# Optimization experiments

Hardware: AMD Instinct MI355X
Metric: run time of the kernel (lower is better)

## Reference

```python
import jax, jax.numpy as jnp
import numpy as np

HIDDEN = 4096
N_HEADS = 32
N_KV_HEADS = 8
HEAD_DIM = 128
ROPE_THETA = 1e6
RMS_EPS = 1e-6
SEQ = 2048


def setup_inputs() -> dict:
    key = jax.random.key(0)
    k1, k2, k3 = jax.random.split(key, 3)
    hidden_states = jax.random.normal(k1, (SEQ, HIDDEN), dtype=jnp.float32)
    # fused QKV weight: [hidden, (H + 2*Hkv) * head_dim]
    qkv_out = (N_HEADS + 2 * N_KV_HEADS) * HEAD_DIM
    w_qkv = jax.random.normal(k2, (HIDDEN, qkv_out), dtype=jnp.float32) * (HIDDEN ** -0.5)
    w_o = jax.random.normal(k3, (N_HEADS * HEAD_DIM, HIDDEN), dtype=jnp.float32) * ((N_HEADS * HEAD_DIM) ** -0.5)
    q_norm_w = jnp.ones((HEAD_DIM,), dtype=jnp.float32)
    k_norm_w = jnp.ones((HEAD_DIM,), dtype=jnp.float32)
    # NeoX-style rotary tables [T, head_dim/2]
    pos = jnp.arange(SEQ, dtype=jnp.float32)
    inv_freq = 1.0 / (ROPE_THETA ** (jnp.arange(0, HEAD_DIM, 2, dtype=jnp.float32) / HEAD_DIM))
    freqs = pos[:, None] * inv_freq[None, :]  # [T, d/2]
    cos = jnp.cos(freqs)
    sin = jnp.sin(freqs)
    return {"hidden_states": hidden_states, "cos": cos, "sin": sin,
            "w_qkv": w_qkv, "w_o": w_o, "q_norm_w": q_norm_w, "k_norm_w": k_norm_w}


def _rms_norm(x, w, eps=RMS_EPS):
    # per-head RMSNorm over last dim (head_dim)
    var = jnp.mean(jnp.square(x), axis=-1, keepdims=True)
    return x * jax.lax.rsqrt(var + eps) * w


def _rope(x, cos, sin):
    # NeoX rotate-half: x split into two halves of head_dim
    d2 = x.shape[-1] // 2
    x1, x2 = x[..., :d2], x[..., d2:]
    c = cos[:, None, :]  # [T,1,d/2] broadcast over heads
    s = sin[:, None, :]
    return jnp.concatenate([x1 * c - x2 * s, x2 * c + x1 * s], axis=-1)


def reference(hidden_states, cos, sin, w_qkv, w_o, q_norm_w, k_norm_w):
    T = hidden_states.shape[0]
    H, Hkv, D = N_HEADS, N_KV_HEADS, HEAD_DIM
    G = H // Hkv  # GQA group size
    scale = D ** -0.5

    qkv = hidden_states @ w_qkv  # [T, (H+2Hkv)*D]
    q, k, v = jnp.split(qkv, [H * D, (H + Hkv) * D], axis=1)
    q = q.reshape(T, H, D)
    k = k.reshape(T, Hkv, D)
    v = v.reshape(T, Hkv, D)

    q = _rms_norm(q, q_norm_w)
    k = _rms_norm(k, k_norm_w)
    q = _rope(q, cos, sin)
    k = _rope(k, cos, sin)

    # GQA: group query heads onto shared KV heads
    qg = q.reshape(T, Hkv, G, D)
    scores = jnp.einsum('qhgd,khd->hgqk', qg, k) * scale  # [Hkv,G,T,T]
    causal = jnp.tril(jnp.ones((T, T), dtype=bool))
    scores = jnp.where(causal, scores, jnp.float32(-1e30))
    probs = jax.nn.softmax(scores, axis=-1)
    out = jnp.einsum('hgqk,khd->qhgd', probs, v).reshape(T, H * D)
    return out @ w_o  # [T, hidden]
```

## Files before the change

kernel.cpp:

```cpp
#include <hip/hip_runtime.h>
#include <stdint.h>

#define SEQ   2048
#define HID   4096
#define NQH   32
#define NKVH  8
#define HD    128
#define QKVN  6144

typedef uint16_t u16;
typedef __attribute__((ext_vector_type(8))) short bf16x8;
typedef __attribute__((ext_vector_type(4))) float f32x4;
typedef __attribute__((ext_vector_type(4))) unsigned int u32x4;

static __device__ __forceinline__ float bf2f(u16 h){
  union { float f; unsigned int u; } v; v.u = ((unsigned int)h) << 16; return v.f;
}
static __device__ __forceinline__ u16 f2bf(float f){
  unsigned int u = __float_as_uint(f);
  return (u16)((u + 0x7fffu + ((u >> 16) & 1u)) >> 16);
}
static __device__ __forceinline__ f32x4 mfma16(bf16x8 a, bf16x8 b, f32x4 c){
  return __builtin_amdgcn_mfma_f32_16x16x32_bf16(a, b, c, 0, 0, 0);
}
static __device__ __forceinline__ void gload16(const void* g, void* l){
  __builtin_amdgcn_global_load_lds((const __attribute__((address_space(1))) void*)g,
                                   (__attribute__((address_space(3))) void*)l, 16, 0, 0);
}

__global__ void k_cvt(const float* __restrict__ src, u16* __restrict__ dst, int n4){
  int i = blockIdx.x * blockDim.x + threadIdx.x;
  if (i >= n4) return;
  float4 v = ((const float4*)src)[i];
  uint2 o;
  o.x = (unsigned)f2bf(v.x) | ((unsigned)f2bf(v.y) << 16);
  o.y = (unsigned)f2bf(v.z) | ((unsigned)f2bf(v.w) << 16);
  ((uint2*)dst)[i] = o;
}

__global__ void k_addf(const float* __restrict__ a, float* __restrict__ o, int n4){
  int i = blockIdx.x * blockDim.x + threadIdx.x;
  if (i >= n4) return;
  float4 x = ((const float4*)o)[i];
  float4 y = ((const float4*)a)[i];
  x.x += y.x; x.y += y.y; x.z += y.z; x.w += y.w;
  ((float4*)o)[i] = x;
}

__global__ void k_transpose_cvt(const float* __restrict__ src, u16* __restrict__ dst, int K, int N){
  __shared__ float t[32][33];
  int n0 = blockIdx.x * 32, k0 = blockIdx.y * 32;
  int tx = threadIdx.x, ty = threadIdx.y;
#pragma unroll
  for (int i = 0; i < 32; i += 8)
    t[ty + i][tx] = src[(size_t)(k0 + ty + i) * N + n0 + tx];
  __syncthreads();
#pragma unroll
  for (int i = 0; i < 32; i += 8)
    dst[(size_t)(n0 + ty + i) * K + k0 + tx] = f2bf(t[tx][ty + i]);
}

template<int OUTBF, int SPLITK, int XBC, int NBY>
__global__ __launch_bounds__(512) void k_gemm(const u16* __restrict__ A, const u16* __restrict__ Bt,
                                              void* __restrict__ Cv0, void* __restrict__ Cv1,
                                              int M, int N, int K){
  __shared__ __align__(16) u16 Asm[2][256][64];
  __shared__ __align__(16) u16 Bsm[2][256][64];
  const int tid = threadIdx.x, lane = tid & 63, wid = tid >> 6;
  const int wm = wid >> 2, wn = wid & 3;
  const int l16 = lane & 15, lhi = lane >> 4;
  const int rx = l16 & 7;
  const int bid = blockIdx.x;
  const int xcd = bid & 7, j = bid >> 3;
  const int bcol_i = xcd * XBC + j % XBC;
  const int rest = j / XBC;
  const int brow_i = rest % NBY;
  const int kz = (SPLITK > 1) ? (rest / NBY) : 0;
  const size_t brow = (size_t)brow_i * 256, bcol = (size_t)bcol_i * 256;
  const int kbeg = kz * (K / SPLITK);
  void* Cv = (kz == 0) ? Cv0 : Cv1;

  const f32x4 vz = {0.f, 0.f, 0.f, 0.f};
  f32x4 acc[8][4];
#pragma unroll
  for (int m = 0; m < 8; m++)
#pragma unroll
    for (int n = 0; n < 4; n++) acc[m][n] = vz;

  const int srow = lane >> 3;
  const int sg   = (lane & 7) ^ srow;
  const u16* Ags = A  + (brow + wid*8 + srow) * (size_t)K + sg*8 + kbeg;
  const u16* Bgs = Bt + (bcol + wid*8 + srow) * (size_t)K + sg*8 + kbeg;
  const int NT = (K / SPLITK) >> 6;

#pragma unroll
  for (int j2 = 0; j2 < 4; j2++) gload16(Ags + (size_t)j2*64*K, &Asm[0][wid*8 + j2*64][0]);
#pragma unroll
  for (int j2 = 0; j2 < 4; j2++) gload16(Bgs + (size_t)j2*64*K, &Bsm[0][wid*8 + j2*64][0]);
  asm volatile("s_waitcnt vmcnt(0)" ::: "memory");
  __builtin_amdgcn_sched_barrier(0);
  __builtin_amdgcn_s_barrier();

  for (int t = 0; t < NT; ++t){
    const int cur = t & 1, nxt = cur ^ 1;
    const size_t ko = (size_t)(t + 1) * 64;
    const bool st = (t + 1 < NT);
    bf16x8 a[8], b0, b1, b2, b3;
#pragma unroll
    for (int mi = 0; mi < 8; ++mi)
      a[mi] = *(const bf16x8*)&Asm[cur][wm*128 + mi*16 + l16][(lhi ^ rx) << 3];
    b0 = *(const bf16x8*)&Bsm[cur][wn*64 +  0 + l16][(lhi ^ rx) << 3];
    b1 = *(const bf16x8*)&Bsm[cur][wn*64 + 16 + l16][(lhi ^ rx) << 3];
    if (st){
      gload16(Ags + ko,                  &Asm[nxt][wid*8      ][0]);
      gload16(Ags + (size_t)64*K + ko,   &Asm[nxt][wid*8 +  64][0]);
      gload16(Bgs + ko,                  &Bsm[nxt][wid*8      ][0]);
      gload16(Bgs + (size_t)64*K + ko,   &Bsm[nxt][wid*8 +  64][0]);
    }
    __builtin_amdgcn_s_barrier();
    asm volatile("s_waitcnt lgkmcnt(0)" ::: "memory");
    __builtin_amdgcn_sched_barrier(0);
    __builtin_amdgcn_s_setprio(1);
#pragma unroll
    for (int mi = 0; mi < 8; ++mi){
      acc[mi][0] = mfma16(a[mi], b0, acc[mi][0]);
      acc[mi][1] = mfma16(a[mi], b1, acc[mi][1]);
    }
    __builtin_amdgcn_s_setprio(0);
    __builtin_amdgcn_s_barrier();
    b2 = *(const bf16x8*)&Bsm[cur][wn*64 + 32 + l16][(lhi ^ rx) << 3];
    b3 = *(const bf16x8*)&Bsm[cur][wn*64 + 48 + l16][(lhi ^ rx) << 3];
    if (st){
      gload16(Ags + (size_t)128*K + ko,  &Asm[nxt][wid*8 + 128][0]);
      gload16(Ags + (size_t)192*K + ko,  &Asm[nxt][wid*8 + 192][0]);
      gload16(Bgs + (size_t)128*K + ko,  &Bsm[nxt][wid*8 + 128][0]);
      gload16(Bgs + (size_t)192*K + ko,  &Bsm[nxt][wid*8 + 192][0]);
    }
    __builtin_amdgcn_s_barrier();
    asm volatile("s_waitcnt lgkmcnt(0)" ::: "memory");
    __builtin_amdgcn_sched_barrier(0);
    __builtin_amdgcn_s_setprio(1);
#pragma unroll
    for (int mi = 0; mi < 8; ++mi){
      acc[mi][2] = mfma16(a[mi], b2, acc[mi][2]);
      acc[mi][3] = mfma16(a[mi], b3, acc[mi][3]);
    }
    __builtin_amdgcn_s_setprio(0);
    __builtin_amdgcn_s_barrier();
#pragma unroll
    for (int mi = 0; mi < 8; ++mi)
      a[mi] = *(const bf16x8*)&Asm[cur][wm*128 + mi*16 + l16][((4 + lhi) ^ rx) << 3];
    b0 = *(const bf16x8*)&Bsm[cur][wn*64 +  0 + l16][((4 + lhi) ^ rx) << 3];
    b1 = *(const bf16x8*)&Bsm[cur][wn*64 + 16 + l16][((4 + lhi) ^ rx) << 3];
    __builtin_amdgcn_s_barrier();
    asm volatile("s_waitcnt lgkmcnt(0)" ::: "memory");
    __builtin_amdgcn_sched_barrier(0);
    __builtin_amdgcn_s_setprio(1);
#pragma unroll
    for (int mi = 0; mi < 8; ++mi){
      acc[mi][0] = mfma16(a[mi], b0, acc[mi][0]);
      acc[mi][1] = mfma16(a[mi], b1, acc[mi][1]);
    }
    __builtin_amdgcn_s_setprio(0);
    __builtin_amdgcn_s_barrier();
    b2 = *(const bf16x8*)&Bsm[cur][wn*64 + 32 + l16][((4 + lhi) ^ rx) << 3];
    b3 = *(const bf16x8*)&Bsm[cur][wn*64 + 48 + l16][((4 + lhi) ^ rx) << 3];
    __builtin_amdgcn_s_barrier();
    asm volatile("s_waitcnt lgkmcnt(0)" ::: "memory");
    __builtin_amdgcn_sched_barrier(0);
    __builtin_amdgcn_s_setprio(1);
#pragma unroll
    for (int mi = 0; mi < 8; ++mi){
      acc[mi][2] = mfma16(a[mi], b2, acc[mi][2]);
      acc[mi][3] = mfma16(a[mi], b3, acc[mi][3]);
    }
    __builtin_amdgcn_s_setprio(0);
    if (st){
      asm volatile("s_waitcnt vmcnt(0)" ::: "memory");
      __builtin_amdgcn_sched_barrier(0);
    }
    __builtin_amdgcn_s_barrier();
  }

#pragma unroll
  for (int mi = 0; mi < 8; mi++)
#pragma unroll
    for (int ni = 0; ni < 4; ni++)
#pragma unroll
      for (int i = 0; i < 4; i++){
        size_t row = brow + wm*128 + mi*16 + lhi*4 + i;
        size_t col = bcol + wn*64 + ni*16 + l16;
        if (OUTBF) ((u16*)Cv)[row * (size_t)N + col] = f2bf(acc[mi][ni][i]);
        else       ((float*)Cv)[row * (size_t)N + col] = acc[mi][ni][i];
      }
}

__global__ __launch_bounds__(256) void k_rmsrope(const u16* __restrict__ qkv, const float* __restrict__ cosp,
                                                 const float* __restrict__ sinp, const float* __restrict__ qw,
                                                 const float* __restrict__ kw, u16* __restrict__ Qr,
                                                 u16* __restrict__ Kr){
  int t = blockIdx.x;
  int lane = threadIdx.x & 63, w = threadIdx.x >> 6;
  int hh = blockIdx.y * 4 + w;
  bool isq = hh < NQH;
  int hl = isq ? hh : hh - NQH;
  const u16* src = qkv + (size_t)t * QKVN + (isq ? hl * HD : NQH * HD + hl * HD);
  unsigned u = *(const unsigned*)(src + 2 * lane);
  float x0 = bf2f((u16)(u & 0xffffu)), x1 = bf2f((u16)(u >> 16));
  float ss = x0 * x0 + x1 * x1;
#pragma unroll
  for (int m = 1; m < 64; m <<= 1) ss += __shfl_xor(ss, m);
  float rs = rsqrtf(ss * (1.f / HD) + 1e-6f);
  const float* wp = isq ? qw : kw;
  float w0 = wp[2 * lane], w1 = wp[2 * lane + 1];
  float xn0 = x0 * rs * w0, xn1 = x1 * rs * w1;
  float p0 = __shfl_xor(xn0, 32), p1 = __shfl_xor(xn1, 32);
  int j0 = (2 * lane) & 63;
  float c0 = cosp[t * 64 + j0], c1 = cosp[t * 64 + j0 + 1];
  float s0 = sinp[t * 64 + j0], s1 = sinp[t * 64 + j0 + 1];
  float o0, o1;
  if (lane < 32){ o0 = xn0 * c0 - p0 * s0; o1 = xn1 * c1 - p1 * s1; }
  else          { o0 = xn0 * c0 + p0 * s0; o1 = xn1 * c1 + p1 * s1; }
  if (isq){ o0 *= 0.08838834764831845f; o1 *= 0.08838834764831845f; }
  u16* dst = isq ? (Qr + ((size_t)hl * SEQ + t) * HD) : (Kr + ((size_t)hl * SEQ + t) * HD);
  *(unsigned*)(dst + 2 * lane) = (unsigned)f2bf(o0) | ((unsigned)f2bf(o1) << 16);
}

__global__ void k_vt(const u16* __restrict__ qkv, u16* __restrict__ VT){
  __shared__ u16 t[32][33];
  int t0 = blockIdx.x * 32, d0 = blockIdx.y * 32, hv = blockIdx.z;
  int tx = threadIdx.x, ty = threadIdx.y;
#pragma unroll
  for (int i = 0; i < 32; i += 8)
    t[ty + i][tx] = qkv[(size_t)(t0 + ty + i) * QKVN + (NQH + NKVH) * HD + hv * HD + d0 + tx];
  __syncthreads();
#pragma unroll
  for (int i = 0; i < 32; i += 8)
    VT[((size_t)hv * HD + d0 + ty + i) * SEQ + t0 + tx] = t[tx][ty + i];
}

__global__ __launch_bounds__(512, 2) void k_attn(const u16* __restrict__ Q, const u16* __restrict__ Kg,
                                                 const u16* __restrict__ VTg, u16* __restrict__ AO){
  __shared__ __align__(16) u16 Ksm[2][64][128];
  __shared__ __align__(16) u16 Vsm[2][128][64];
  __shared__ __align__(16) u16 Psm[8][16][72];
  int tid = threadIdx.x, lane = tid & 63, wid = tid >> 6;
  int l16 = lane & 15, lhi = lane >> 4;
  int bid = blockIdx.x;
  int kvg = bid & 7, rr = bid >> 3;
  int J = 15 - (rr >> 2);
  int hq = kvg * 4 + (rr & 3);
  int qb = J * 128;
  const u16* Kh = Kg  + (size_t)kvg * SEQ * HD;
  const u16* Vh = VTg + (size_t)kvg * HD * SEQ;
  const u16* Qh = Q   + (size_t)hq * SEQ * HD;

  bf16x8 qf[4];
#pragma unroll
  for (int ks = 0; ks < 4; ks++)
    qf[ks] = *(const bf16x8*)(Qh + (size_t)(qb + wid*16 + l16) * HD + ks*32 + lhi*8);

  const f32x4 vz = {0.f, 0.f, 0.f, 0.f};
  f32x4 o[8];
  float mrow[4], lrow[4];
#pragma unroll
  for (int n = 0; n < 8; n++) o[n] = vz;
#pragma unroll
  for (int i = 0; i < 4; i++){ mrow[i] = -1e30f; lrow[i] = 0.f; }

  int krl0 = wid*8 + (lane >> 4), krl1 = krl0 + 4;
  int kgs  = lane & 15;
  const u16* ks0 = Kh + (size_t)krl0 * HD + ((kgs ^ (krl0 & 7)) << 3);
  const u16* ks1 = Kh + (size_t)krl1 * HD + ((kgs ^ (krl1 & 7)) << 3);
  int vrl0 = wid*16 + (lane >> 3), vrl1 = vrl0 + 8;
  int vgs  = lane & 7;
  const u16* vs0 = Vh + (size_t)vrl0 * SEQ + ((vgs ^ (vrl0 & 7)) << 3);
  const u16* vs1 = Vh + (size_t)vrl1 * SEQ + ((vgs ^ (vrl1 & 7)) << 3);

  gload16(ks0, &Ksm[0][wid*8][0]);
  gload16(ks1, &Ksm[0][wid*8 + 4][0]);
  gload16(vs0, &Vsm[0][wid*16][0]);
  gload16(vs1, &Vsm[0][wid*16 + 8][0]);
  __syncthreads();

  int ntr = 2*J + 2;
  int wrow0 = qb + wid*16;
  for (int t = 0; t < ntr; t++){
    int cur = t & 1, nxt = cur ^ 1;
    int kt0 = t << 6;
    if (t < ntr - 1){
      size_t ko = (size_t)(t + 1) * 64 * HD;
      gload16(ks0 + ko, &Ksm[nxt][wid*8][0]);
      gload16(ks1 + ko, &Ksm[nxt][wid*8 + 4][0]);
      int vo = (t + 1) * 64;
      gload16(vs0 + vo, &Vsm[nxt][wid*16][0]);
      gload16(vs1 + vo, &Vsm[nxt][wid*16 + 8][0]);
    }
    if (kt0 <= wrow0 + 15){
      f32x4 s[4];
#pragma unroll
      for (int n = 0; n < 4; n++) s[n] = vz;
      const u16* kbase = &Ksm[cur][0][0];
#pragma unroll
      for (int n = 0; n < 4; n++){
        int row = n*16 + l16, rxk = row & 7;
#pragma unroll
        for (int ks = 0; ks < 4; ks++){
          bf16x8 kf = *(const bf16x8*)(kbase + row*128 + (((ks*4 + lhi) ^ rxk) << 3));
          s[n] = mfma16(qf[ks], kf, s[n]);
        }
      }
      if (kt0 + 63 > wrow0){
#pragma unroll
        for (int n = 0; n < 4; n++)
#pragma unroll
          for (int i = 0; i < 4; i++)
            if (kt0 + n*16 + l16 > wrow0 + lhi*4 + i) s[n][i] = -1e30f;
      }
#pragma unroll
      for (int i = 0; i < 4; i++){
        float tm = fmaxf(fmaxf(s[0][i], s[1][i]), fmaxf(s[2][i], s[3][i]));
        tm = fmaxf(tm, __shfl_xor(tm, 1));
        tm = fmaxf(tm, __shfl_xor(tm, 2));
        tm = fmaxf(tm, __shfl_xor(tm, 4));
        tm = fmaxf(tm, __shfl_xor(tm, 8));
        float nm = fmaxf(mrow[i], tm);
        float sc = __expf(mrow[i] - nm);
        mrow[i] = nm;
        float rsum = 0.f;
#pragma unroll
        for (int n = 0; n < 4; n++){
          float p = __expf(s[n][i] - nm);
          s[n][i] = p;
          rsum += p;
        }
        rsum += __shfl_xor(rsum, 1);
        rsum += __shfl_xor(rsum, 2);
        rsum += __shfl_xor(rsum, 4);
        rsum += __shfl_xor(rsum, 8);
        lrow[i] = lrow[i] * sc + rsum;
#pragma unroll
        for (int n = 0; n < 8; n++) o[n][i] *= sc;
      }
#pragma unroll
      for (int n = 0; n < 4; n++)
#pragma unroll
        for (int i = 0; i < 4; i++)
          Psm[wid][lhi*4 + i][n*16 + l16] = f2bf(s[n][i]);
      const u16* vbase = &Vsm[cur][0][0];
#pragma unroll
      for (int ksv = 0; ksv < 2; ksv++){
        bf16x8 pa = *(const bf16x8*)&Psm[wid][l16][ksv*32 + lhi*8];
#pragma unroll
        for (int n = 0; n < 8; n++){
          int row = n*16 + l16;
          bf16x8 vb = *(const bf16x8*)(vbase + row*64 + ((((ksv*4) + lhi) ^ (row & 7)) << 3));
          o[n] = mfma16(pa, vb, o[n]);
        }
      }
    }
    if (t < ntr - 1) __syncthreads();
  }
  float inv[4];
#pragma unroll
  for (int i = 0; i < 4; i++) inv[i] = 1.f / lrow[i];
#pragma unroll
  for (int n = 0; n < 8; n++)
#pragma unroll
    for (int i = 0; i < 4; i++){
      int trow = wrow0 + lhi*4 + i;
      AO[(size_t)trow * HID + hq * HD + n*16 + l16] = f2bf(o[n][i] * inv[i]);
    }
}

extern "C" void kernel_launch(void* const* d_in, const int* in_sizes, int n_in,
                              void* d_out, int out_size, void* d_ws, size_t ws_size,
                              hipStream_t stream){
  const float* hs   = (const float*)d_in[0];
  const float* cosp = (const float*)d_in[1];
  const float* sinp = (const float*)d_in[2];
  const float* wqkv = (const float*)d_in[3];
  const float* wo   = (const float*)d_in[4];
  const float* qw   = (const float*)d_in[5];
  const float* kw   = (const float*)d_in[6];
  float* out = (float*)d_out;
  char* ws = (char*)d_ws;
  u16* XB    = (u16*)(ws + 0);
  u16* WQKVT = (u16*)(ws + 16777216);
  u16* WOT   = (u16*)(ws + 0);
  float* SCR = (float*)(ws + 33554432);
  u16* QKV   = (u16*)(ws + 67108864);
  u16* QR    = (u16*)(ws + 92274688);
  u16* KR    = (u16*)(ws + 109051904);
  u16* VTB   = (u16*)(ws + 113246208);
  u16* AOB   = (u16*)(ws + 117440512);

  k_cvt<<<(SEQ * HID / 4 + 255) / 256, 256, 0, stream>>>(hs, XB, SEQ * HID / 4);
  k_transpose_cvt<<<dim3(QKVN / 32, HID / 32), dim3(32, 8), 0, stream>>>(wqkv, WQKVT, HID, QKVN);
  k_gemm<1, 1, 3, 8><<<192, 512, 0, stream>>>(XB, WQKVT, QKV, nullptr, SEQ, QKVN, HID);
  k_transpose_cvt<<<dim3(HID / 32, HID / 32), dim3(32, 8), 0, stream>>>(wo, WOT, HID, HID);
  k_rmsrope<<<dim3(SEQ, 10), 256, 0, stream>>>(QKV, cosp, sinp, qw, kw, QR, KR);
  k_vt<<<dim3(SEQ / 32, HD / 32, NKVH), dim3(32, 8), 0, stream>>>(QKV, VTB);
  k_attn<<<512, 512, 0, stream>>>(QR, KR, VTB, AOB);
  k_gemm<0, 2, 2, 8><<<256, 512, 0, stream>>>(AOB, WOT, out, SCR, SEQ, HID, HID);
  k_addf<<<SEQ * HID / 4 / 256, 256, 0, stream>>>(SCR, out, SEQ * HID / 4);
}
```

Measured before the change: 369.4 us.

## Widen attention KV tiles to 128 and split K/V load pipeline

Result: faster. 358.3 us (-3.0%).

```diff
diff --git a/kernel.cpp b/kernel.cpp
--- a/kernel.cpp
+++ b/kernel.cpp
@@ -239,11 +239,11 @@
     VT[((size_t)hv * HD + d0 + ty + i) * SEQ + t0 + tx] = t[tx][ty + i];
 }
 
-__global__ __launch_bounds__(512, 2) void k_attn(const u16* __restrict__ Q, const u16* __restrict__ Kg,
-                                                 const u16* __restrict__ VTg, u16* __restrict__ AO){
-  __shared__ __align__(16) u16 Ksm[2][64][128];
-  __shared__ __align__(16) u16 Vsm[2][128][64];
-  __shared__ __align__(16) u16 Psm[8][16][72];
+__global__ __launch_bounds__(512) void k_attn(const u16* __restrict__ Q, const u16* __restrict__ Kg,
+                                              const u16* __restrict__ VTg, u16* __restrict__ AO){
+  __shared__ __align__(16) u16 Ksm[2][128][128];
+  __shared__ __align__(16) u16 Vsm[128][128];
+  __shared__ __align__(16) u16 Psm[8][16][136];
   int tid = threadIdx.x, lane = tid & 63, wid = tid >> 6;
   int l16 = lane & 15, lhi = lane >> 4;
   int bid = blockIdx.x;
@@ -268,98 +268,119 @@
 #pragma unroll
   for (int i = 0; i < 4; i++){ mrow[i] = -1e30f; lrow[i] = 0.f; }
 
-  int krl0 = wid*8 + (lane >> 4), krl1 = krl0 + 4;
-  int kgs  = lane & 15;
-  const u16* ks0 = Kh + (size_t)krl0 * HD + ((kgs ^ (krl0 & 7)) << 3);
-  const u16* ks1 = Kh + (size_t)krl1 * HD + ((kgs ^ (krl1 & 7)) << 3);
-  int vrl0 = wid*16 + (lane >> 3), vrl1 = vrl0 + 8;
-  int vgs  = lane & 7;
-  const u16* vs0 = Vh + (size_t)vrl0 * SEQ + ((vgs ^ (vrl0 & 7)) << 3);
-  const u16* vs1 = Vh + (size_t)vrl1 * SEQ + ((vgs ^ (vrl1 & 7)) << 3);
-
-  gload16(ks0, &Ksm[0][wid*8][0]);
-  gload16(ks1, &Ksm[0][wid*8 + 4][0]);
-  gload16(vs0, &Vsm[0][wid*16][0]);
-  gload16(vs1, &Vsm[0][wid*16 + 8][0]);
-  __syncthreads();
-
-  int ntr = 2*J + 2;
+  int rsub = lane >> 4, g = lane & 15;
+  const u16 *Ks0, *Ks1, *Ks2, *Ks3, *Vs0, *Vs1, *Vs2, *Vs3;
+  {
+    int r0 = wid*16 + 0*4 + rsub, r1 = wid*16 + 1*4 + rsub;
+    int r2 = wid*16 + 2*4 + rsub, r3 = wid*16 + 3*4 + rsub;
+    Ks0 = Kh + (size_t)r0 * HD + ((g ^ (r0 & 7)) << 3);
+    Ks1 = Kh + (size_t)r1 * HD + ((g ^ (r1 & 7)) << 3);
+    Ks2 = Kh + (size_t)r2 * HD + ((g ^ (r2 & 7)) << 3);
+    Ks3 = Kh + (size_t)r3 * HD + ((g ^ (r3 & 7)) << 3);
+    Vs0 = Vh + (size_t)r0 * SEQ + ((g ^ (r0 & 7)) << 3);
+    Vs1 = Vh + (size_t)r1 * SEQ + ((g ^ (r1 & 7)) << 3);
+    Vs2 = Vh + (size_t)r2 * SEQ + ((g ^ (r2 & 7)) << 3);
+    Vs3 = Vh + (size_t)r3 * SEQ + ((g ^ (r3 & 7)) << 3);
+  }
+
+  gload16(Ks0, &Ksm[0][wid*16 +  0][0]);
+  gload16(Ks1, &Ksm[0][wid*16 +  4][0]);
+  gload16(Ks2, &Ksm[0][wid*16 +  8][0]);
+  gload16(Ks3, &Ksm[0][wid*16 + 12][0]);
+  asm volatile("s_waitcnt vmcnt(0)" ::: "memory");
+  __builtin_amdgcn_sched_barrier(0);
+  __builtin_amdgcn_s_barrier();
+
+  int ntr = J + 1;
   int wrow0 = qb + wid*16;
   for (int t = 0; t < ntr; t++){
     int cur = t & 1, nxt = cur ^ 1;
-    int kt0 = t << 6;
-    if (t < ntr - 1){
-      size_t ko = (size_t)(t + 1) * 64 * HD;
-      gload16(ks0 + ko, &Ksm[nxt][wid*8][0]);
-      gload16(ks1 + ko, &Ksm[nxt][wid*8 + 4][0]);
-      int vo = (t + 1) * 64;
-      gload16(vs0 + vo, &Vsm[nxt][wid*16][0]);
-      gload16(vs1 + vo, &Vsm[nxt][wid*16 + 8][0]);
-    }
-    if (kt0 <= wrow0 + 15){
-      f32x4 s[4];
-#pragma unroll
-      for (int n = 0; n < 4; n++) s[n] = vz;
-      const u16* kbase = &Ksm[cur][0][0];
-#pragma unroll
-      for (int n = 0; n < 4; n++){
-        int row = n*16 + l16, rxk = row & 7;
-#pragma unroll
-        for (int ks = 0; ks < 4; ks++){
-          bf16x8 kf = *(const bf16x8*)(kbase + row*128 + (((ks*4 + lhi) ^ rxk) << 3));
-          s[n] = mfma16(qf[ks], kf, s[n]);
-        }
+    int kt0 = t << 7;
+    bool pf = (t + 1 < ntr);
+    gload16(Vs0 + kt0, &Vsm[wid*16 +  0][0]);
+    gload16(Vs1 + kt0, &Vsm[wid*16 +  4][0]);
+    gload16(Vs2 + kt0, &Vsm[wid*16 +  8][0]);
+    gload16(Vs3 + kt0, &Vsm[wid*16 + 12][0]);
+    if (pf){
+      size_t ko = (size_t)(kt0 + 128) * HD;
+      gload16(Ks0 + ko, &Ksm[nxt][wid*16 +  0][0]);
+      gload16(Ks1 + ko, &Ksm[nxt][wid*16 +  4][0]);
+      gload16(Ks2 + ko, &Ksm[nxt][wid*16 +  8][0]);
+      gload16(Ks3 + ko, &Ksm[nxt][wid*16 + 12][0]);
+    }
+    f32x4 s[8];
+#pragma unroll
+    for (int n = 0; n < 8; n++) s[n] = vz;
+    const u16* kbase = &Ksm[cur][0][0];
+    __builtin_amdgcn_s_setprio(1);
+#pragma unroll
+    for (int n = 0; n < 8; n++){
+      int row = n*16 + l16, rxk = row & 7;
+#pragma unroll
+      for (int ks = 0; ks < 4; ks++){
+        bf16x8 kf = *(const bf16x8*)(kbase + row*128 + (((ks*4 + lhi) ^ rxk) << 3));
+        s[n] = mfma16(qf[ks], kf, s[n]);
       }
-      if (kt0 + 63 > wrow0){
-#pragma unroll
-        for (int n = 0; n < 4; n++)
-#pragma unroll
-          for (int i = 0; i < 4; i++)
-            if (kt0 + n*16 + l16 > wrow0 + lhi*4 + i) s[n][i] = -1e30f;
+    }
+    __builtin_amdgcn_s_setprio(0);
+    if (kt0 + 127 > wrow0){
+#pragma unroll
+      for (int n = 0; n < 8; n++)
+#pragma unroll
+        for (int i = 0; i < 4; i++)
+          if (kt0 + n*16 + l16 > wrow0 + lhi*4 + i) s[n][i] = -1e30f;
+    }
+#pragma unroll
+    for (int i = 0; i < 4; i++){
+      float tm = fmaxf(fmaxf(fmaxf(s[0][i], s[1][i]), fmaxf(s[2][i], s[3][i])),
+                       fmaxf(fmaxf(s[4][i], s[5][i]), fmaxf(s[6][i], s[7][i])));
+      tm = fmaxf(tm, __shfl_xor(tm, 1));
+      tm = fmaxf(tm, __shfl_xor(tm, 2));
+      tm = fmaxf(tm, __shfl_xor(tm, 4));
+      tm = fmaxf(tm, __shfl_xor(tm, 8));
+      float nm = fmaxf(mrow[i], tm);
+      float sc = __expf(mrow[i] - nm);
+      mrow[i] = nm;
+      float rsum = 0.f;
+#pragma unroll
+      for (int n = 0; n < 8; n++){
+        float p = __expf(s[n][i] - nm);
+        s[n][i] = p;
+        rsum += p;
       }
-#pragma unroll
-      for (int i = 0; i < 4; i++){
-        float tm = fmaxf(fmaxf(s[0][i], s[1][i]), fmaxf(s[2][i], s[3][i]));
-        tm = fmaxf(tm, __shfl_xor(tm, 1));
-        tm = fmaxf(tm, __shfl_xor(tm, 2));
-        tm = fmaxf(tm, __shfl_xor(tm, 4));
-        tm = fmaxf(tm, __shfl_xor(tm, 8));
-        float nm = fmaxf(mrow[i], tm);
-        float sc = __expf(mrow[i] - nm);
-        mrow[i] = nm;
-        float rsum = 0.f;
-#pragma unroll
-        for (int n = 0; n < 4; n++){
-          float p = __expf(s[n][i] - nm);
-          s[n][i] = p;
-          rsum += p;
-        }
-        rsum += __shfl_xor(rsum, 1);
-        rsum += __shfl_xor(rsum, 2);
-        rsum += __shfl_xor(rsum, 4);
-        rsum += __shfl_xor(rsum, 8);
-        lrow[i] = lrow[i] * sc + rsum;
-#pragma unroll
-        for (int n = 0; n < 8; n++) o[n][i] *= sc;
+      rsum += __shfl_xor(rsum, 1);
+      rsum += __shfl_xor(rsum, 2);
+      rsum += __shfl_xor(rsum, 4);
+      rsum += __shfl_xor(rsum, 8);
+      lrow[i] = lrow[i] * sc + rsum;
+#pragma unroll
+      for (int n = 0; n < 8; n++) o[n][i] *= sc;
+    }
+#pragma unroll
+    for (int n = 0; n < 8; n++)
+#pragma unroll
+      for (int i = 0; i < 4; i++)
+        Psm[wid][lhi*4 + i][n*16 + l16] = f2bf(s[n][i]);
+    if (pf) asm volatile("s_waitcnt vmcnt(4)" ::: "memory");
+    else    asm volatile("s_waitcnt vmcnt(0)" ::: "memory");
+    __builtin_amdgcn_sched_barrier(0);
+    __builtin_amdgcn_s_barrier();
+    __builtin_amdgcn_sched_barrier(0);
+    __builtin_amdgcn_s_setprio(1);
+#pragma unroll
+    for (int ksv = 0; ksv < 4; ksv++){
+      bf16x8 pa = *(const bf16x8*)&Psm[wid][l16][ksv*32 + lhi*8];
+#pragma unroll
+      for (int n = 0; n < 8; n++){
+        int row = n*16 + l16;
+        bf16x8 vb = *(const bf16x8*)(&Vsm[0][0] + row*128 + (((ksv*4 + lhi) ^ (row & 7)) << 3));
+        o[n] = mfma16(pa, vb, o[n]);
       }
-#pragma unroll
-      for (int n = 0; n < 4; n++)
-#pragma unroll
-        for (int i = 0; i < 4; i++)
-          Psm[wid][lhi*4 + i][n*16 + l16] = f2bf(s[n][i]);
-      const u16* vbase = &Vsm[cur][0][0];
-#pragma unroll
-      for (int ksv = 0; ksv < 2; ksv++){
-        bf16x8 pa = *(const bf16x8*)&Psm[wid][l16][ksv*32 + lhi*8];
-#pragma unroll
-        for (int n = 0; n < 8; n++){
-          int row = n*16 + l16;
-          bf16x8 vb = *(const bf16x8*)(vbase + row*64 + ((((ksv*4) + lhi) ^ (row & 7)) << 3));
-          o[n] = mfma16(pa, vb, o[n]);
-        }
-      }
-    }
-    if (t < ntr - 1) __syncthreads();
+    }
+    __builtin_amdgcn_s_setprio(0);
+    asm volatile("s_waitcnt vmcnt(0)" ::: "memory");
+    __builtin_amdgcn_sched_barrier(0);
+    __builtin_amdgcn_s_barrier();
   }
   float inv[4];
 #pragma unroll
```
